# Performance work log

Hardware: AMD Instinct MI355X
Metric: run time of the kernel (lower is better)

Reference implementation:

```python
import jax, jax.numpy as jnp
import numpy as np

BS, P, MAX_GT, C_IN, NCLS = 16, 4096, 32, 512, 4


def _make_boxes(key, shape):
    k1, k2, k3, k4 = jax.random.split(key, 4)
    x0 = jax.random.uniform(k1, shape) * 500.0
    y0 = jax.random.uniform(k2, shape) * 500.0
    w = 10.0 + jax.random.uniform(k3, shape) * 90.0
    h = 10.0 + jax.random.uniform(k4, shape) * 90.0
    return jnp.stack([x0, y0, x0 + w, y0 + h], -1)


def setup_inputs() -> dict:
    key = jax.random.key(0)
    ks = jax.random.split(key, 10)
    v = jax.random.normal(ks[0], (BS * P, C_IN), jnp.float32)
    rois = _make_boxes(ks[1], (BS, P))
    gt_boxes = _make_boxes(ks[2], (BS, MAX_GT))
    gt_counts = jax.random.randint(ks[3], (BS,), 0, MAX_GT + 1, jnp.int32)
    lab_idx = jax.random.randint(ks[4], (BS,), 0, NCLS)
    labels = jax.nn.one_hot(lab_idx, NCLS, dtype=jnp.float32)
    pre_score = jax.random.uniform(ks[5], (BS, P, NCLS), dtype=jnp.float32)
    cls_w = jax.random.normal(ks[6], (NCLS, C_IN), jnp.float32) * 0.01
    cls_b = jnp.full((NCLS,), -np.log((1.0 - 0.01) / 0.01), jnp.float32)
    reg_w = jax.random.normal(ks[7], (NCLS, C_IN), jnp.float32) * 0.01
    reg_b = jnp.zeros((NCLS,), jnp.float32)
    return {"v": v, "gt_boxes": gt_boxes, "gt_counts": gt_counts, "rois": rois,
            "labels": labels, "pre_score": pre_score, "cls_w": cls_w,
            "cls_b": cls_b, "reg_w": reg_w, "reg_b": reg_b}


def _box_iou(a, b):
    # a: (bs, Na, 4), b: (bs, Nb, 4) -> (bs, Na, Nb)
    area_a = (a[..., 2] - a[..., 0]) * (a[..., 3] - a[..., 1])
    area_b = (b[..., 2] - b[..., 0]) * (b[..., 3] - b[..., 1])
    lt = jnp.maximum(a[..., :, None, :2], b[..., None, :, :2])
    rb = jnp.minimum(a[..., :, None, 2:], b[..., None, :, 2:])
    wh = jnp.clip(rb - lt, 0.0)
    inter = wh[..., 0] * wh[..., 1]
    return inter / (area_a[..., :, None] + area_b[..., None, :] - inter)


def _ce(logits, tgt3):
    # CrossEntropyLoss(reduction='none'): logsumexp - logit[target]
    return jax.nn.logsumexp(logits, -1) - jnp.take_along_axis(logits, tgt3, -1)[..., 0]


def _smooth_l1(x):
    ax = jnp.abs(x)
    return jnp.where(ax < 1.0, 0.5 * ax * ax, ax - 0.5)


def reference(v, gt_boxes, gt_counts, rois, labels, pre_score, cls_w, cls_b, reg_w, reg_b):
    bs, Pn = rois.shape[:2]
    classify = (v @ cls_w.T + cls_b).reshape(bs, Pn, NCLS)
    reg = (v @ reg_w.T + reg_b).reshape(bs, Pn, NCLS)
    label = jnp.argmax(labels, 1)                                  # (bs,)
    lbl3 = jnp.broadcast_to(label[:, None, None], (bs, Pn, 1))

    # background branch: CE on raw logits, mean over proposals
    ce_bg = _ce(classify, lbl3).mean(1)                            # (bs,)

    # foreground branch: CE on clamped logits weighted by pre_score
    c = jnp.clip(classify, 1e-7, 1.0 - 1e-7)
    ps = jnp.take_along_axis(pre_score, lbl3, 2)[..., 0]           # (bs, P)
    ce_fg = _ce(c, lbl3) * ps

    gt_valid = jnp.arange(MAX_GT)[None, :] < gt_counts[:, None]    # (bs, MAX_GT)
    ious = _box_iou(gt_boxes, rois)                                # (bs, MAX_GT, P)
    ious = jnp.where(gt_valid[:, :, None], ious, -1.0)
    mask = jnp.any(ious > 0.5, 1).astype(classify.dtype)           # (bs, P)
    c_fg = (ce_fg * mask).sum(1) / (mask.sum(1) + 1e-7)

    idx = jnp.argmax(ious, 1)                                      # (bs, P)
    g = jnp.take_along_axis(gt_boxes, jnp.broadcast_to(idx[:, :, None], (bs, Pn, 4)), 1)
    gx = (g[..., 2] + g[..., 0]) / 2; gy = (g[..., 3] + g[..., 1]) / 2
    gw = (g[..., 2] - g[..., 0]) / 2; gh = (g[..., 3] - g[..., 1]) / 2
    r = rois
    rx = (r[..., 2] + r[..., 0]) / 2; ry = (r[..., 3] + r[..., 1]) / 2
    rw = (r[..., 2] - r[..., 0]) / 2; rh = (r[..., 3] - r[..., 1]) / 2
    tx = (gx - rx) / (rw + 1e-8); ty = (gy - ry) / (rh + 1e-8)
    tw = jnp.log(gw / (rw + 1e-8)); th = jnp.log(gh / (rh + 1e-8))
    t = jnp.stack([tx, ty, tw, th], -1)                            # (bs, P, 4)
    l1 = (_smooth_l1(reg - t).sum(-1) * mask * ps).sum(1) / (bs * Pn)

    has_gt = gt_counts > 0
    c_list = jnp.where(has_gt, c_fg, 0.0).sum()
    c_bg = jnp.where(has_gt, 0.0, ce_bg).sum()
    bg = jnp.where(has_gt, 0.0, float(Pn)).sum()
    l1_list = jnp.where(has_gt, l1, 0.0).sum()
    return (c_list + c_bg / (bg + 1e-7)) / (bs + 1e-7) + l1_list
```

## Files before the change

### kernel.cpp

```cpp
#include <hip/hip_runtime.h>
#include <math.h>

#define BSZ 16
#define NP 4096
#define MAXGT 32
#define CIN 512
#define NCLS 4
#define PB 64
#define NBLK (BSZ * NP / PB)
#define BPB (NP / PB)

__global__ __launch_bounds__(256, 4) void oicr_main(
    const float* __restrict__ v,
    const float* __restrict__ gt_boxes,
    const int*   __restrict__ gt_counts,
    const float* __restrict__ rois,
    const float* __restrict__ labels,
    const float* __restrict__ pre_score,
    const float* __restrict__ cls_w,
    const float* __restrict__ cls_b,
    const float* __restrict__ reg_w,
    const float* __restrict__ reg_b,
    float* __restrict__ partials)
{
    __shared__ float w8[8][CIN];
    __shared__ float red8[4][PB][9];
    __shared__ float s_bias[8];
    __shared__ float g_x0[MAXGT], g_y0[MAXGT], g_x1[MAXGT], g_y1[MAXGT];
    __shared__ float g_area[MAXGT];
    __shared__ int   g_valid[MAXGT];
    __shared__ int   s_label;

    const int tid  = threadIdx.x;
    const int lane = tid & 63;
    const int wv   = tid >> 6;
    const int b    = blockIdx.x >> 6;
    const int p    = (blockIdx.x & 63) * PB + lane;
    const int row  = b * NP + p;

    #pragma unroll
    for (int i = tid; i < 8 * CIN; i += 256) {
        int c = i >> 9, k = i & (CIN - 1);
        w8[c][k] = (c < 4) ? cls_w[c * CIN + k] : reg_w[(c - 4) * CIN + k];
    }
    if (tid < 8) s_bias[tid] = (tid < 4) ? cls_b[tid] : reg_b[tid - 4];
    if (tid < MAXGT) {
        int cnt = gt_counts[b];
        const float* g = gt_boxes + (size_t)(b * MAXGT + tid) * 4;
        float x0 = g[0], y0 = g[1], x1 = g[2], y1 = g[3];
        g_x0[tid] = x0; g_y0[tid] = y0; g_x1[tid] = x1; g_y1[tid] = y1;
        g_area[tid] = (x1 - x0) * (y1 - y0);
        g_valid[tid] = (tid < cnt) ? 1 : 0;
    }
    if (tid == 0) {
        const float* L = labels + b * NCLS;
        int bi = 0; float bv = L[0];
        #pragma unroll
        for (int c = 1; c < NCLS; ++c) { if (L[c] > bv) { bv = L[c]; bi = c; } }
        s_label = bi;
    }
    __syncthreads();

    const int kq = __builtin_amdgcn_readfirstlane(wv);
    float acc[8];
    #pragma unroll
    for (int c = 0; c < 8; ++c) acc[c] = 0.f;

    const float4* vrow = (const float4*)(v + (size_t)row * CIN) + kq * 32;
    #pragma unroll 8
    for (int i = 0; i < 32; ++i) {
        float4 a = vrow[i];
        const int k = (kq * 32 + i) * 4;
        #pragma unroll
        for (int c = 0; c < 8; ++c) {
            float4 w4 = *(const float4*)&w8[c][k];
            acc[c] += a.x * w4.x + a.y * w4.y + a.z * w4.z + a.w * w4.w;
        }
    }

    #pragma unroll
    for (int c = 0; c < 8; ++c) red8[wv][lane][c] = acc[c];
    __syncthreads();

    if (wv != 0) return;

    #pragma unroll
    for (int c = 0; c < 8; ++c)
        acc[c] = red8[0][lane][c] + red8[1][lane][c] +
                 red8[2][lane][c] + red8[3][lane][c];

    const float cls0 = acc[0] + s_bias[0];
    const float cls1 = acc[1] + s_bias[1];
    const float cls2 = acc[2] + s_bias[2];
    const float cls3 = acc[3] + s_bias[3];
    const float reg0 = acc[4] + s_bias[4];
    const float reg1 = acc[5] + s_bias[5];
    const float reg2 = acc[6] + s_bias[6];
    const float reg3 = acc[7] + s_bias[7];

    const int lbl = s_label;

    float mB = fmaxf(fmaxf(cls0, cls1), fmaxf(cls2, cls3));
    float lseB = mB + logf(expf(cls0 - mB) + expf(cls1 - mB) +
                           expf(cls2 - mB) + expf(cls3 - mB));
    float clsL = (lbl == 0) ? cls0 : (lbl == 1) ? cls1 : (lbl == 2) ? cls2 : cls3;
    float ce_bg = lseB - clsL;

    const float lo = 1e-7f, hi = 1.f - 1e-7f;
    float cc0 = fminf(fmaxf(cls0, lo), hi);
    float cc1 = fminf(fmaxf(cls1, lo), hi);
    float cc2 = fminf(fmaxf(cls2, lo), hi);
    float cc3 = fminf(fmaxf(cls3, lo), hi);
    float mF = fmaxf(fmaxf(cc0, cc1), fmaxf(cc2, cc3));
    float lseF = mF + logf(expf(cc0 - mF) + expf(cc1 - mF) +
                           expf(cc2 - mF) + expf(cc3 - mF));
    float ccL = (lbl == 0) ? cc0 : (lbl == 1) ? cc1 : (lbl == 2) ? cc2 : cc3;
    float ce_fg = lseF - ccL;
    float ps = pre_score[(size_t)row * NCLS + lbl];

    float4 r = *(const float4*)(rois + (size_t)row * 4);
    float rarea = (r.z - r.x) * (r.w - r.y);
    float best = -3.0e38f;
    int   bi = 0;
    int   mk = 0;
    #pragma unroll
    for (int g = 0; g < MAXGT; ++g) {
        float ix0 = fmaxf(r.x, g_x0[g]);
        float iy0 = fmaxf(r.y, g_y0[g]);
        float ix1 = fminf(r.z, g_x1[g]);
        float iy1 = fminf(r.w, g_y1[g]);
        float iw = fmaxf(ix1 - ix0, 0.f);
        float ih = fmaxf(iy1 - iy0, 0.f);
        float inter = iw * ih;
        float iou = inter / (g_area[g] + rarea - inter);
        iou = g_valid[g] ? iou : -1.0f;
        if (iou > best) { best = iou; bi = g; }
        mk |= (iou > 0.5f) ? 1 : 0;
    }
    float maskf = mk ? 1.f : 0.f;

    float gx0 = g_x0[bi], gy0 = g_y0[bi], gx1 = g_x1[bi], gy1 = g_y1[bi];
    float gx = (gx1 + gx0) * 0.5f, gy = (gy1 + gy0) * 0.5f;
    float gw = (gx1 - gx0) * 0.5f, gh = (gy1 - gy0) * 0.5f;
    float rx = (r.z + r.x) * 0.5f, ry = (r.w + r.y) * 0.5f;
    float rw = (r.z - r.x) * 0.5f, rh = (r.w - r.y) * 0.5f;
    float tx = (gx - rx) / (rw + 1e-8f);
    float ty = (gy - ry) / (rh + 1e-8f);
    float tw = logf(gw / (rw + 1e-8f));
    float th = logf(gh / (rh + 1e-8f));

    float d0 = reg0 - tx, d1 = reg1 - ty, d2 = reg2 - tw, d3 = reg3 - th;
    float a0 = fabsf(d0), a1 = fabsf(d1), a2 = fabsf(d2), a3 = fabsf(d3);
    float s0 = (a0 < 1.f) ? 0.5f * a0 * a0 : a0 - 0.5f;
    float s1 = (a1 < 1.f) ? 0.5f * a1 * a1 : a1 - 0.5f;
    float s2 = (a2 < 1.f) ? 0.5f * a2 * a2 : a2 - 0.5f;
    float s3 = (a3 < 1.f) ? 0.5f * a3 * a3 : a3 - 0.5f;
    float sl1 = s0 + s1 + s2 + s3;

    float px = ce_bg;
    float py = ce_fg * ps * maskf;
    float pz = maskf;
    float pw = sl1 * maskf * ps;

    #pragma unroll
    for (int off = 32; off > 0; off >>= 1) {
        px += __shfl_down(px, off);
        py += __shfl_down(py, off);
        pz += __shfl_down(pz, off);
        pw += __shfl_down(pw, off);
    }
    if (lane == 0) {
        partials[(size_t)blockIdx.x * 4 + 0] = px;
        partials[(size_t)blockIdx.x * 4 + 1] = py;
        partials[(size_t)blockIdx.x * 4 + 2] = pz;
        partials[(size_t)blockIdx.x * 4 + 3] = pw;
    }
}

__global__ __launch_bounds__(64) void oicr_final(
    const float* __restrict__ partials,
    const int*   __restrict__ gt_counts,
    float* __restrict__ out)
{
    const int lane = threadIdx.x;
    float S0 = 0.f, S1 = 0.f, S2 = 0.f, S3 = 0.f;
    float c_term = 0.f, cbg_term = 0.f, bg_term = 0.f, l1_term = 0.f;
    if (lane < BSZ) {
        for (int blk = 0; blk < BPB; ++blk) {
            const float* q = partials + (size_t)(lane * BPB + blk) * 4;
            S0 += q[0]; S1 += q[1]; S2 += q[2]; S3 += q[3];
        }
        bool has = gt_counts[lane] > 0;
        float c_fg       = S1 / (S2 + 1e-7f);
        float ce_bg_mean = S0 / (float)NP;
        float l1b        = S3 / (float)(BSZ * NP);
        c_term   = has ? c_fg : 0.f;
        cbg_term = has ? 0.f : ce_bg_mean;
        bg_term  = has ? 0.f : (float)NP;
        l1_term  = has ? l1b : 0.f;
    }
    #pragma unroll
    for (int off = 32; off > 0; off >>= 1) {
        c_term   += __shfl_down(c_term, off);
        cbg_term += __shfl_down(cbg_term, off);
        bg_term  += __shfl_down(bg_term, off);
        l1_term  += __shfl_down(l1_term, off);
    }
    if (lane == 0) {
        out[0] = (c_term + cbg_term / (bg_term + 1e-7f)) / ((float)BSZ + 1e-7f)
                 + l1_term;
    }
}

extern "C" void kernel_launch(void* const* d_in, const int* in_sizes, int n_in,
                              void* d_out, int out_size, void* d_ws, size_t ws_size,
                              hipStream_t stream)
{
    const float* v         = (const float*)d_in[0];
    const float* gt_boxes  = (const float*)d_in[1];
    const int*   gt_counts = (const int*)  d_in[2];
    const float* rois      = (const float*)d_in[3];
    const float* labels    = (const float*)d_in[4];
    const float* pre_score = (const float*)d_in[5];
    const float* cls_w     = (const float*)d_in[6];
    const float* cls_b     = (const float*)d_in[7];
    const float* reg_w     = (const float*)d_in[8];
    const float* reg_b     = (const float*)d_in[9];
    float* out      = (float*)d_out;
    float* partials = (float*)d_ws;

    oicr_main<<<dim3(NBLK), dim3(256), 0, stream>>>(
        v, gt_boxes, gt_counts, rois, labels, pre_score,
        cls_w, cls_b, reg_w, reg_b, partials);
    oicr_final<<<dim3(1), dim3(64), 0, stream>>>(partials, gt_counts, out);
}
```

Measured before the change: 46.69 us.

## Process two rows per thread and read weights directly instead of staging in LDS

Each block now handles 128 proposals, with every thread computing two rows. Weight vectors are loaded once per k-step from global/L1 and reused across both rows, and the 16 KB shared-memory weight staging plus its barrier are removed. This halves the block count and the per-block weight-load overhead, at the cost of more registers (launch bounds lowered to 2 blocks per SIMD) and uniform global weight loads in the inner loop.

```diff
diff --git a/kernel.cpp b/kernel.cpp
--- a/kernel.cpp
+++ b/kernel.cpp
@@ -6,11 +6,12 @@
 #define MAXGT 32
 #define CIN 512
 #define NCLS 4
-#define PB 64
+#define RPT 2
+#define PB (64 * RPT)
 #define NBLK (BSZ * NP / PB)
 #define BPB (NP / PB)
 
-__global__ __launch_bounds__(256, 4) void oicr_main(
+__global__ __launch_bounds__(256, 2) void oicr_main(
     const float* __restrict__ v,
     const float* __restrict__ gt_boxes,
     const int*   __restrict__ gt_counts,
@@ -23,7 +24,6 @@
     const float* __restrict__ reg_b,
     float* __restrict__ partials)
 {
-    __shared__ float w8[8][CIN];
     __shared__ float red8[4][PB][9];
     __shared__ float s_bias[8];
     __shared__ float g_x0[MAXGT], g_y0[MAXGT], g_x1[MAXGT], g_y1[MAXGT];
@@ -31,18 +31,14 @@
     __shared__ int   g_valid[MAXGT];
     __shared__ int   s_label;
 
-    const int tid  = threadIdx.x;
-    const int lane = tid & 63;
-    const int wv   = tid >> 6;
-    const int b    = blockIdx.x >> 6;
-    const int p    = (blockIdx.x & 63) * PB + lane;
-    const int row  = b * NP + p;
-
-    #pragma unroll
-    for (int i = tid; i < 8 * CIN; i += 256) {
-        int c = i >> 9, k = i & (CIN - 1);
-        w8[c][k] = (c < 4) ? cls_w[c * CIN + k] : reg_w[(c - 4) * CIN + k];
-    }
+    const int tid   = threadIdx.x;
+    const int lane  = tid & 63;
+    const int wv    = tid >> 6;
+    const int b     = blockIdx.x >> 5;
+    const int pbase = (blockIdx.x & 31) * PB;
+    const int row0  = b * NP + pbase + lane;
+    const int row1  = row0 + 64;
+
     if (tid < 8) s_bias[tid] = (tid < 4) ? cls_b[tid] : reg_b[tid - 4];
     if (tid < MAXGT) {
         int cnt = gt_counts[b];
@@ -59,108 +55,126 @@
         for (int c = 1; c < NCLS; ++c) { if (L[c] > bv) { bv = L[c]; bi = c; } }
         s_label = bi;
     }
-    __syncthreads();
 
     const int kq = __builtin_amdgcn_readfirstlane(wv);
-    float acc[8];
-    #pragma unroll
-    for (int c = 0; c < 8; ++c) acc[c] = 0.f;
-
-    const float4* vrow = (const float4*)(v + (size_t)row * CIN) + kq * 32;
+    float acc0[8], acc1[8];
+    #pragma unroll
+    for (int c = 0; c < 8; ++c) { acc0[c] = 0.f; acc1[c] = 0.f; }
+
+    const float4* vr0 = (const float4*)(v + (size_t)row0 * CIN) + kq * 32;
+    const float4* vr1 = (const float4*)(v + (size_t)row1 * CIN) + kq * 32;
+
     #pragma unroll 8
     for (int i = 0; i < 32; ++i) {
-        float4 a = vrow[i];
+        float4 a0 = vr0[i];
+        float4 a1 = vr1[i];
         const int k = (kq * 32 + i) * 4;
         #pragma unroll
-        for (int c = 0; c < 8; ++c) {
-            float4 w4 = *(const float4*)&w8[c][k];
-            acc[c] += a.x * w4.x + a.y * w4.y + a.z * w4.z + a.w * w4.w;
+        for (int c = 0; c < 4; ++c) {
+            float4 wc = *(const float4*)&cls_w[c * CIN + k];
+            float4 wr = *(const float4*)&reg_w[c * CIN + k];
+            acc0[c]     += a0.x * wc.x + a0.y * wc.y + a0.z * wc.z + a0.w * wc.w;
+            acc1[c]     += a1.x * wc.x + a1.y * wc.y + a1.z * wc.z + a1.w * wc.w;
+            acc0[4 + c] += a0.x * wr.x + a0.y * wr.y + a0.z * wr.z + a0.w * wr.w;
+            acc1[4 + c] += a1.x * wr.x + a1.y * wr.y + a1.z * wr.z + a1.w * wr.w;
         }
     }
 
     #pragma unroll
-    for (int c = 0; c < 8; ++c) red8[wv][lane][c] = acc[c];
+    for (int c = 0; c < 8; ++c) {
+        red8[wv][lane][c]      = acc0[c];
+        red8[wv][64 + lane][c] = acc1[c];
+    }
     __syncthreads();
 
     if (wv != 0) return;
 
-    #pragma unroll
-    for (int c = 0; c < 8; ++c)
-        acc[c] = red8[0][lane][c] + red8[1][lane][c] +
-                 red8[2][lane][c] + red8[3][lane][c];
-
-    const float cls0 = acc[0] + s_bias[0];
-    const float cls1 = acc[1] + s_bias[1];
-    const float cls2 = acc[2] + s_bias[2];
-    const float cls3 = acc[3] + s_bias[3];
-    const float reg0 = acc[4] + s_bias[4];
-    const float reg1 = acc[5] + s_bias[5];
-    const float reg2 = acc[6] + s_bias[6];
-    const float reg3 = acc[7] + s_bias[7];
-
-    const int lbl = s_label;
-
-    float mB = fmaxf(fmaxf(cls0, cls1), fmaxf(cls2, cls3));
-    float lseB = mB + logf(expf(cls0 - mB) + expf(cls1 - mB) +
-                           expf(cls2 - mB) + expf(cls3 - mB));
-    float clsL = (lbl == 0) ? cls0 : (lbl == 1) ? cls1 : (lbl == 2) ? cls2 : cls3;
-    float ce_bg = lseB - clsL;
-
-    const float lo = 1e-7f, hi = 1.f - 1e-7f;
-    float cc0 = fminf(fmaxf(cls0, lo), hi);
-    float cc1 = fminf(fmaxf(cls1, lo), hi);
-    float cc2 = fminf(fmaxf(cls2, lo), hi);
-    float cc3 = fminf(fmaxf(cls3, lo), hi);
-    float mF = fmaxf(fmaxf(cc0, cc1), fmaxf(cc2, cc3));
-    float lseF = mF + logf(expf(cc0 - mF) + expf(cc1 - mF) +
-                           expf(cc2 - mF) + expf(cc3 - mF));
-    float ccL = (lbl == 0) ? cc0 : (lbl == 1) ? cc1 : (lbl == 2) ? cc2 : cc3;
-    float ce_fg = lseF - ccL;
-    float ps = pre_score[(size_t)row * NCLS + lbl];
-
-    float4 r = *(const float4*)(rois + (size_t)row * 4);
-    float rarea = (r.z - r.x) * (r.w - r.y);
-    float best = -3.0e38f;
-    int   bi = 0;
-    int   mk = 0;
-    #pragma unroll
-    for (int g = 0; g < MAXGT; ++g) {
-        float ix0 = fmaxf(r.x, g_x0[g]);
-        float iy0 = fmaxf(r.y, g_y0[g]);
-        float ix1 = fminf(r.z, g_x1[g]);
-        float iy1 = fminf(r.w, g_y1[g]);
-        float iw = fmaxf(ix1 - ix0, 0.f);
-        float ih = fmaxf(iy1 - iy0, 0.f);
-        float inter = iw * ih;
-        float iou = inter / (g_area[g] + rarea - inter);
-        iou = g_valid[g] ? iou : -1.0f;
-        if (iou > best) { best = iou; bi = g; }
-        mk |= (iou > 0.5f) ? 1 : 0;
-    }
-    float maskf = mk ? 1.f : 0.f;
-
-    float gx0 = g_x0[bi], gy0 = g_y0[bi], gx1 = g_x1[bi], gy1 = g_y1[bi];
-    float gx = (gx1 + gx0) * 0.5f, gy = (gy1 + gy0) * 0.5f;
-    float gw = (gx1 - gx0) * 0.5f, gh = (gy1 - gy0) * 0.5f;
-    float rx = (r.z + r.x) * 0.5f, ry = (r.w + r.y) * 0.5f;
-    float rw = (r.z - r.x) * 0.5f, rh = (r.w - r.y) * 0.5f;
-    float tx = (gx - rx) / (rw + 1e-8f);
-    float ty = (gy - ry) / (rh + 1e-8f);
-    float tw = logf(gw / (rw + 1e-8f));
-    float th = logf(gh / (rh + 1e-8f));
-
-    float d0 = reg0 - tx, d1 = reg1 - ty, d2 = reg2 - tw, d3 = reg3 - th;
-    float a0 = fabsf(d0), a1 = fabsf(d1), a2 = fabsf(d2), a3 = fabsf(d3);
-    float s0 = (a0 < 1.f) ? 0.5f * a0 * a0 : a0 - 0.5f;
-    float s1 = (a1 < 1.f) ? 0.5f * a1 * a1 : a1 - 0.5f;
-    float s2 = (a2 < 1.f) ? 0.5f * a2 * a2 : a2 - 0.5f;
-    float s3 = (a3 < 1.f) ? 0.5f * a3 * a3 : a3 - 0.5f;
-    float sl1 = s0 + s1 + s2 + s3;
-
-    float px = ce_bg;
-    float py = ce_fg * ps * maskf;
-    float pz = maskf;
-    float pw = sl1 * maskf * ps;
+    float px = 0.f, py = 0.f, pz = 0.f, pw = 0.f;
+
+    #pragma unroll
+    for (int rr = 0; rr < RPT; ++rr) {
+        const int li  = rr * 64 + lane;
+        const int row = row0 + rr * 64;
+
+        float acc[8];
+        #pragma unroll
+        for (int c = 0; c < 8; ++c)
+            acc[c] = red8[0][li][c] + red8[1][li][c] +
+                     red8[2][li][c] + red8[3][li][c];
+
+        const float cls0 = acc[0] + s_bias[0];
+        const float cls1 = acc[1] + s_bias[1];
+        const float cls2 = acc[2] + s_bias[2];
+        const float cls3 = acc[3] + s_bias[3];
+        const float reg0 = acc[4] + s_bias[4];
+        const float reg1 = acc[5] + s_bias[5];
+        const float reg2 = acc[6] + s_bias[6];
+        const float reg3 = acc[7] + s_bias[7];
+
+        const int lbl = s_label;
+
+        float mB = fmaxf(fmaxf(cls0, cls1), fmaxf(cls2, cls3));
+        float lseB = mB + logf(expf(cls0 - mB) + expf(cls1 - mB) +
+                               expf(cls2 - mB) + expf(cls3 - mB));
+        float clsL = (lbl == 0) ? cls0 : (lbl == 1) ? cls1 : (lbl == 2) ? cls2 : cls3;
+        float ce_bg = lseB - clsL;
+
+        const float lo = 1e-7f, hi = 1.f - 1e-7f;
+        float cc0 = fminf(fmaxf(cls0, lo), hi);
+        float cc1 = fminf(fmaxf(cls1, lo), hi);
+        float cc2 = fminf(fmaxf(cls2, lo), hi);
+        float cc3 = fminf(fmaxf(cls3, lo), hi);
+        float mF = fmaxf(fmaxf(cc0, cc1), fmaxf(cc2, cc3));
+        float lseF = mF + logf(expf(cc0 - mF) + expf(cc1 - mF) +
+                               expf(cc2 - mF) + expf(cc3 - mF));
+        float ccL = (lbl == 0) ? cc0 : (lbl == 1) ? cc1 : (lbl == 2) ? cc2 : cc3;
+        float ce_fg = lseF - ccL;
+        float ps = pre_score[(size_t)row * NCLS + lbl];
+
+        float4 r = *(const float4*)(rois + (size_t)row * 4);
+        float rarea = (r.z - r.x) * (r.w - r.y);
+        float best = -3.0e38f;
+        int   bi = 0;
+        int   mk = 0;
+        #pragma unroll
+        for (int g = 0; g < MAXGT; ++g) {
+            float ix0 = fmaxf(r.x, g_x0[g]);
+            float iy0 = fmaxf(r.y, g_y0[g]);
+            float ix1 = fminf(r.z, g_x1[g]);
+            float iy1 = fminf(r.w, g_y1[g]);
+            float iw = fmaxf(ix1 - ix0, 0.f);
+            float ih = fmaxf(iy1 - iy0, 0.f);
+            float inter = iw * ih;
+            float iou = inter / (g_area[g] + rarea - inter);
+            iou = g_valid[g] ? iou : -1.0f;
+            if (iou > best) { best = iou; bi = g; }
+            mk |= (iou > 0.5f) ? 1 : 0;
+        }
+        float maskf = mk ? 1.f : 0.f;
+
+        float gx0 = g_x0[bi], gy0 = g_y0[bi], gx1 = g_x1[bi], gy1 = g_y1[bi];
+        float gx = (gx1 + gx0) * 0.5f, gy = (gy1 + gy0) * 0.5f;
+        float gw = (gx1 - gx0) * 0.5f, gh = (gy1 - gy0) * 0.5f;
+        float rx = (r.z + r.x) * 0.5f, ry = (r.w + r.y) * 0.5f;
+        float rw = (r.z - r.x) * 0.5f, rh = (r.w - r.y) * 0.5f;
+        float tx = (gx - rx) / (rw + 1e-8f);
+        float ty = (gy - ry) / (rh + 1e-8f);
+        float tw = logf(gw / (rw + 1e-8f));
+        float th = logf(gh / (rh + 1e-8f));
+
+        float d0 = reg0 - tx, d1 = reg1 - ty, d2 = reg2 - tw, d3 = reg3 - th;
+        float a0 = fabsf(d0), a1 = fabsf(d1), a2 = fabsf(d2), a3 = fabsf(d3);
+        float s0 = (a0 < 1.f) ? 0.5f * a0 * a0 : a0 - 0.5f;
+        float s1 = (a1 < 1.f) ? 0.5f * a1 * a1 : a1 - 0.5f;
+        float s2 = (a2 < 1.f) ? 0.5f * a2 * a2 : a2 - 0.5f;
+        float s3 = (a3 < 1.f) ? 0.5f * a3 * a3 : a3 - 0.5f;
+        float sl1 = s0 + s1 + s2 + s3;
+
+        px += ce_bg;
+        py += ce_fg * ps * maskf;
+        pz += maskf;
+        pw += sl1 * maskf * ps;
+    }
 
     #pragma unroll
     for (int off = 32; off > 0; off >>= 1) {
```

New measurement: 42.68 us. 8.6% less time.

## Stream v tiles into LDS via async global_load_lds double buffering

Applied to the files above, without the earlier changes.

Each block now handles 128 rows. The v matrix is staged through a double-buffered LDS arena using global_load_lds DMA with an XOR swizzle, so the next K-chunk is fetched while the current one is being consumed. Weights are read straight from global memory (cached) instead of being copied into LDS. This aims to get more bytes in flight and better coalescing on the bandwidth-bound v read. In exchange it adds per-stage barriers, a larger LDS footprint and lower occupancy (launch bounds 2).

```diff
diff --git a/kernel.cpp b/kernel.cpp
--- a/kernel.cpp
+++ b/kernel.cpp
@@ -6,11 +6,19 @@
 #define MAXGT 32
 #define CIN 512
 #define NCLS 4
-#define PB 64
-#define NBLK (BSZ * NP / PB)
-#define BPB (NP / PB)
-
-__global__ __launch_bounds__(256, 4) void oicr_main(
+#define RPB 128
+#define NBLK (BSZ * NP / RPB)
+#define BPB (NP / RPB)
+
+typedef float f32x4 __attribute__((ext_vector_type(4)));
+
+__device__ __forceinline__ void dma16(const void* g, void* l) {
+    __builtin_amdgcn_global_load_lds(
+        (const __attribute__((address_space(1))) void*)g,
+        (__attribute__((address_space(3))) void*)l, 16, 0, 0);
+}
+
+__global__ __launch_bounds__(256, 2) void oicr_main(
     const float* __restrict__ v,
     const float* __restrict__ gt_boxes,
     const int*   __restrict__ gt_counts,
@@ -23,26 +31,22 @@
     const float* __restrict__ reg_b,
     float* __restrict__ partials)
 {
-    __shared__ float w8[8][CIN];
-    __shared__ float red8[4][PB][9];
+    __shared__ __align__(16) char arena[2][32768];
     __shared__ float s_bias[8];
     __shared__ float g_x0[MAXGT], g_y0[MAXGT], g_x1[MAXGT], g_y1[MAXGT];
     __shared__ float g_area[MAXGT];
     __shared__ int   g_valid[MAXGT];
     __shared__ int   s_label;
+    __shared__ float red2[2][4];
 
     const int tid  = threadIdx.x;
     const int lane = tid & 63;
     const int wv   = tid >> 6;
-    const int b    = blockIdx.x >> 6;
-    const int p    = (blockIdx.x & 63) * PB + lane;
-    const int row  = b * NP + p;
-
-    #pragma unroll
-    for (int i = tid; i < 8 * CIN; i += 256) {
-        int c = i >> 9, k = i & (CIN - 1);
-        w8[c][k] = (c < 4) ? cls_w[c * CIN + k] : reg_w[(c - 4) * CIN + k];
-    }
+    const int kw   = __builtin_amdgcn_readfirstlane(wv);
+    const int blk  = blockIdx.x;
+    const int b    = blk >> 5;
+    const int row0 = blk * RPB;
+
     if (tid < 8) s_bias[tid] = (tid < 4) ? cls_b[tid] : reg_b[tid - 4];
     if (tid < MAXGT) {
         int cnt = gt_counts[b];
@@ -59,121 +63,164 @@
         for (int c = 1; c < NCLS; ++c) { if (L[c] > bv) { bv = L[c]; bi = c; } }
         s_label = bi;
     }
+
+    #define STAGE(P, BB) do {                                                  \
+        const int h_ = (P) & 1, kq_ = (P) >> 1;                                \
+        const char* gb_ = (const char*)v +                                     \
+            ((size_t)(row0 + h_ * 64) * CIN + (size_t)kq_ * 128) * 4;          \
+        char* lb_ = &arena[BB][0] + kw * 8192;                                 \
+        _Pragma("unroll")                                                      \
+        for (int pp_ = 0; pp_ < 8; ++pp_) {                                    \
+            const int D_ = kw * 8192 + pp_ * 1024 + lane * 16;                 \
+            const int F_ = D_ ^ (((D_ >> 9) & 7) << 4);                        \
+            const int rf_ = F_ >> 9, ko_ = F_ & 511;                           \
+            dma16(gb_ + (size_t)rf_ * (CIN * 4) + ko_, lb_ + pp_ * 1024);      \
+        }                                                                      \
+    } while (0)
+
+    float accA[8], accB[8];
+    #pragma unroll
+    for (int c = 0; c < 8; ++c) { accA[c] = 0.f; accB[c] = 0.f; }
+
+    STAGE(0, 0);
     __syncthreads();
 
-    const int kq = __builtin_amdgcn_readfirstlane(wv);
-    float acc[8];
-    #pragma unroll
-    for (int c = 0; c < 8; ++c) acc[c] = 0.f;
-
-    const float4* vrow = (const float4*)(v + (size_t)row * CIN) + kq * 32;
-    #pragma unroll 8
-    for (int i = 0; i < 32; ++i) {
-        float4 a = vrow[i];
-        const int k = (kq * 32 + i) * 4;
-        #pragma unroll
-        for (int c = 0; c < 8; ++c) {
-            float4 w4 = *(const float4*)&w8[c][k];
-            acc[c] += a.x * w4.x + a.y * w4.y + a.z * w4.z + a.w * w4.w;
-        }
-    }
-
-    #pragma unroll
-    for (int c = 0; c < 8; ++c) red8[wv][lane][c] = acc[c];
+    #pragma unroll
+    for (int p = 0; p < 8; ++p) {
+        if (p < 7) STAGE(p + 1, (p + 1) & 1);
+        const int kq = p >> 1;
+        const char* bp = &arena[p & 1][0];
+        #pragma unroll
+        for (int j = 0; j < 8; ++j) {
+            const int A  = lane * 512 + kw * 128 + j * 16;
+            const int As = A ^ ((lane & 7) << 4);
+            f32x4 a = *(const f32x4*)(bp + As);
+            const int k = kq * 128 + kw * 32 + j * 4;
+            #pragma unroll
+            for (int c = 0; c < 4; ++c) {
+                const f32x4 wc = *(const f32x4*)&cls_w[c * CIN + k];
+                const f32x4 wr = *(const f32x4*)&reg_w[c * CIN + k];
+                if ((p & 1) == 0) {
+                    accA[c]     += a[0]*wc[0] + a[1]*wc[1] + a[2]*wc[2] + a[3]*wc[3];
+                    accA[4 + c] += a[0]*wr[0] + a[1]*wr[1] + a[2]*wr[2] + a[3]*wr[3];
+                } else {
+                    accB[c]     += a[0]*wc[0] + a[1]*wc[1] + a[2]*wc[2] + a[3]*wc[3];
+                    accB[4 + c] += a[0]*wr[0] + a[1]*wr[1] + a[2]*wr[2] + a[3]*wr[3];
+                }
+            }
+        }
+        __syncthreads();
+    }
+    #undef STAGE
+
+    float* red8 = (float*)&arena[0][0];
+    #pragma unroll
+    for (int c = 0; c < 8; ++c) {
+        red8[((kw * 128) + lane) * 8 + c]      = accA[c];
+        red8[((kw * 128) + 64 + lane) * 8 + c] = accB[c];
+    }
     __syncthreads();
 
-    if (wv != 0) return;
-
-    #pragma unroll
-    for (int c = 0; c < 8; ++c)
-        acc[c] = red8[0][lane][c] + red8[1][lane][c] +
-                 red8[2][lane][c] + red8[3][lane][c];
-
-    const float cls0 = acc[0] + s_bias[0];
-    const float cls1 = acc[1] + s_bias[1];
-    const float cls2 = acc[2] + s_bias[2];
-    const float cls3 = acc[3] + s_bias[3];
-    const float reg0 = acc[4] + s_bias[4];
-    const float reg1 = acc[5] + s_bias[5];
-    const float reg2 = acc[6] + s_bias[6];
-    const float reg3 = acc[7] + s_bias[7];
-
-    const int lbl = s_label;
-
-    float mB = fmaxf(fmaxf(cls0, cls1), fmaxf(cls2, cls3));
-    float lseB = mB + logf(expf(cls0 - mB) + expf(cls1 - mB) +
-                           expf(cls2 - mB) + expf(cls3 - mB));
-    float clsL = (lbl == 0) ? cls0 : (lbl == 1) ? cls1 : (lbl == 2) ? cls2 : cls3;
-    float ce_bg = lseB - clsL;
-
-    const float lo = 1e-7f, hi = 1.f - 1e-7f;
-    float cc0 = fminf(fmaxf(cls0, lo), hi);
-    float cc1 = fminf(fmaxf(cls1, lo), hi);
-    float cc2 = fminf(fmaxf(cls2, lo), hi);
-    float cc3 = fminf(fmaxf(cls3, lo), hi);
-    float mF = fmaxf(fmaxf(cc0, cc1), fmaxf(cc2, cc3));
-    float lseF = mF + logf(expf(cc0 - mF) + expf(cc1 - mF) +
-                           expf(cc2 - mF) + expf(cc3 - mF));
-    float ccL = (lbl == 0) ? cc0 : (lbl == 1) ? cc1 : (lbl == 2) ? cc2 : cc3;
-    float ce_fg = lseF - ccL;
-    float ps = pre_score[(size_t)row * NCLS + lbl];
-
-    float4 r = *(const float4*)(rois + (size_t)row * 4);
-    float rarea = (r.z - r.x) * (r.w - r.y);
-    float best = -3.0e38f;
-    int   bi = 0;
-    int   mk = 0;
-    #pragma unroll
-    for (int g = 0; g < MAXGT; ++g) {
-        float ix0 = fmaxf(r.x, g_x0[g]);
-        float iy0 = fmaxf(r.y, g_y0[g]);
-        float ix1 = fminf(r.z, g_x1[g]);
-        float iy1 = fminf(r.w, g_y1[g]);
-        float iw = fmaxf(ix1 - ix0, 0.f);
-        float ih = fmaxf(iy1 - iy0, 0.f);
-        float inter = iw * ih;
-        float iou = inter / (g_area[g] + rarea - inter);
-        iou = g_valid[g] ? iou : -1.0f;
-        if (iou > best) { best = iou; bi = g; }
-        mk |= (iou > 0.5f) ? 1 : 0;
-    }
-    float maskf = mk ? 1.f : 0.f;
-
-    float gx0 = g_x0[bi], gy0 = g_y0[bi], gx1 = g_x1[bi], gy1 = g_y1[bi];
-    float gx = (gx1 + gx0) * 0.5f, gy = (gy1 + gy0) * 0.5f;
-    float gw = (gx1 - gx0) * 0.5f, gh = (gy1 - gy0) * 0.5f;
-    float rx = (r.z + r.x) * 0.5f, ry = (r.w + r.y) * 0.5f;
-    float rw = (r.z - r.x) * 0.5f, rh = (r.w - r.y) * 0.5f;
-    float tx = (gx - rx) / (rw + 1e-8f);
-    float ty = (gy - ry) / (rh + 1e-8f);
-    float tw = logf(gw / (rw + 1e-8f));
-    float th = logf(gh / (rh + 1e-8f));
-
-    float d0 = reg0 - tx, d1 = reg1 - ty, d2 = reg2 - tw, d3 = reg3 - th;
-    float a0 = fabsf(d0), a1 = fabsf(d1), a2 = fabsf(d2), a3 = fabsf(d3);
-    float s0 = (a0 < 1.f) ? 0.5f * a0 * a0 : a0 - 0.5f;
-    float s1 = (a1 < 1.f) ? 0.5f * a1 * a1 : a1 - 0.5f;
-    float s2 = (a2 < 1.f) ? 0.5f * a2 * a2 : a2 - 0.5f;
-    float s3 = (a3 < 1.f) ? 0.5f * a3 * a3 : a3 - 0.5f;
-    float sl1 = s0 + s1 + s2 + s3;
-
-    float px = ce_bg;
-    float py = ce_fg * ps * maskf;
-    float pz = maskf;
-    float pw = sl1 * maskf * ps;
-
-    #pragma unroll
-    for (int off = 32; off > 0; off >>= 1) {
-        px += __shfl_down(px, off);
-        py += __shfl_down(py, off);
-        pz += __shfl_down(pz, off);
-        pw += __shfl_down(pw, off);
-    }
-    if (lane == 0) {
-        partials[(size_t)blockIdx.x * 4 + 0] = px;
-        partials[(size_t)blockIdx.x * 4 + 1] = py;
-        partials[(size_t)blockIdx.x * 4 + 2] = pz;
-        partials[(size_t)blockIdx.x * 4 + 3] = pw;
+    float px = 0.f, py = 0.f, pz = 0.f, pw = 0.f;
+    if (tid < 128) {
+        const int row = row0 + tid;
+        float acc[8];
+        #pragma unroll
+        for (int c = 0; c < 8; ++c)
+            acc[c] = red8[(0 * 128 + tid) * 8 + c] + red8[(1 * 128 + tid) * 8 + c]
+                   + red8[(2 * 128 + tid) * 8 + c] + red8[(3 * 128 + tid) * 8 + c];
+
+        const float cls0 = acc[0] + s_bias[0];
+        const float cls1 = acc[1] + s_bias[1];
+        const float cls2 = acc[2] + s_bias[2];
+        const float cls3 = acc[3] + s_bias[3];
+        const float reg0 = acc[4] + s_bias[4];
+        const float reg1 = acc[5] + s_bias[5];
+        const float reg2 = acc[6] + s_bias[6];
+        const float reg3 = acc[7] + s_bias[7];
+
+        const int lbl = s_label;
+
+        float mB = fmaxf(fmaxf(cls0, cls1), fmaxf(cls2, cls3));
+        float lseB = mB + logf(expf(cls0 - mB) + expf(cls1 - mB) +
+                               expf(cls2 - mB) + expf(cls3 - mB));
+        float clsL = (lbl == 0) ? cls0 : (lbl == 1) ? cls1 : (lbl == 2) ? cls2 : cls3;
+        float ce_bg = lseB - clsL;
+
+        const float lo = 1e-7f, hi2 = 1.f - 1e-7f;
+        float cc0 = fminf(fmaxf(cls0, lo), hi2);
+        float cc1 = fminf(fmaxf(cls1, lo), hi2);
+        float cc2 = fminf(fmaxf(cls2, lo), hi2);
+        float cc3 = fminf(fmaxf(cls3, lo), hi2);
+        float mF = fmaxf(fmaxf(cc0, cc1), fmaxf(cc2, cc3));
+        float lseF = mF + logf(expf(cc0 - mF) + expf(cc1 - mF) +
+                               expf(cc2 - mF) + expf(cc3 - mF));
+        float ccL = (lbl == 0) ? cc0 : (lbl == 1) ? cc1 : (lbl == 2) ? cc2 : cc3;
+        float ce_fg = lseF - ccL;
+        float ps = pre_score[(size_t)row * NCLS + lbl];
+
+        float4 r = *(const float4*)(rois + (size_t)row * 4);
+        float rarea = (r.z - r.x) * (r.w - r.y);
+        float best = -3.0e38f;
+        int   bi = 0;
+        int   mk = 0;
+        #pragma unroll
+        for (int g = 0; g < MAXGT; ++g) {
+            float ix0 = fmaxf(r.x, g_x0[g]);
+            float iy0 = fmaxf(r.y, g_y0[g]);
+            float ix1 = fminf(r.z, g_x1[g]);
+            float iy1 = fminf(r.w, g_y1[g]);
+            float iw = fmaxf(ix1 - ix0, 0.f);
+            float ih = fmaxf(iy1 - iy0, 0.f);
+            float inter = iw * ih;
+            float iou = inter / (g_area[g] + rarea - inter);
+            iou = g_valid[g] ? iou : -1.0f;
+            if (iou > best) { best = iou; bi = g; }
+            mk |= (iou > 0.5f) ? 1 : 0;
+        }
+        float maskf = mk ? 1.f : 0.f;
+
+        float gx0 = g_x0[bi], gy0 = g_y0[bi], gx1 = g_x1[bi], gy1 = g_y1[bi];
+        float gx = (gx1 + gx0) * 0.5f, gy = (gy1 + gy0) * 0.5f;
+        float gw = (gx1 - gx0) * 0.5f, gh = (gy1 - gy0) * 0.5f;
+        float rx = (r.z + r.x) * 0.5f, ry = (r.w + r.y) * 0.5f;
+        float rw = (r.z - r.x) * 0.5f, rh = (r.w - r.y) * 0.5f;
+        float tx = (gx - rx) / (rw + 1e-8f);
+        float ty = (gy - ry) / (rh + 1e-8f);
+        float tw = logf(gw / (rw + 1e-8f));
+        float th = logf(gh / (rh + 1e-8f));
+
+        float d0 = reg0 - tx, d1 = reg1 - ty, d2 = reg2 - tw, d3 = reg3 - th;
+        float a0 = fabsf(d0), a1 = fabsf(d1), a2 = fabsf(d2), a3 = fabsf(d3);
+        float s0 = (a0 < 1.f) ? 0.5f * a0 * a0 : a0 - 0.5f;
+        float s1 = (a1 < 1.f) ? 0.5f * a1 * a1 : a1 - 0.5f;
+        float s2 = (a2 < 1.f) ? 0.5f * a2 * a2 : a2 - 0.5f;
+        float s3 = (a3 < 1.f) ? 0.5f * a3 * a3 : a3 - 0.5f;
+        float sl1 = s0 + s1 + s2 + s3;
+
+        px = ce_bg;
+        py = ce_fg * ps * maskf;
+        pz = maskf;
+        pw = sl1 * maskf * ps;
+
+        #pragma unroll
+        for (int off = 32; off > 0; off >>= 1) {
+            px += __shfl_down(px, off);
+            py += __shfl_down(py, off);
+            pz += __shfl_down(pz, off);
+            pw += __shfl_down(pw, off);
+        }
+        if (lane == 0) {
+            red2[wv][0] = px; red2[wv][1] = py;
+            red2[wv][2] = pz; red2[wv][3] = pw;
+        }
+    }
+    __syncthreads();
+    if (tid == 0) {
+        partials[(size_t)blk * 4 + 0] = red2[0][0] + red2[1][0];
+        partials[(size_t)blk * 4 + 1] = red2[0][1] + red2[1][1];
+        partials[(size_t)blk * 4 + 2] = red2[0][2] + red2[1][2];
+        partials[(size_t)blk * 4 + 3] = red2[0][3] + red2[1][3];
     }
 }
 
```

Result: slower. 76.51 us (+63.9%).
